# Performance work log

Measured on AMD Instinct MI355X. Metric: run time of the kernel, lower is better.

## Reference

```python
import jax, jax.numpy as jnp
import numpy as np

NUM_HEADS = 16


def setup_inputs() -> dict:
    key = jax.random.key(0)
    k1, k2, k3 = jax.random.split(key, 3)
    B, N, C = 2, 2048, 1024
    x = jax.random.normal(k1, (B, N, C), dtype=jnp.float32)
    w_qkv = jax.random.normal(k2, (3 * C, C), dtype=jnp.float32) * (C ** -0.5)
    w_proj = jax.random.normal(k3, (C, C), dtype=jnp.float32) * (C ** -0.5)
    b_proj = jnp.zeros((C,), dtype=jnp.float32)
    return {"x": x, "w_qkv": w_qkv, "w_proj": w_proj, "b_proj": b_proj}


def reference(x, w_qkv, w_proj, b_proj):
    B, N, C = x.shape
    H = NUM_HEADS
    D = C // H
    scale = 1.0 / jnp.sqrt(jnp.asarray(D, x.dtype))
    qkv = (x @ w_qkv.T).reshape(B, N, 3, H, D)
    qkv = jnp.transpose(qkv, (2, 0, 3, 1, 4))  # [3,B,H,N,D]
    q, k, v = qkv[0], qkv[1], qkv[2]
    # scaled dot-product attention with explicit score matrix [B,H,N,N]
    attn = jnp.einsum('bhnd,bhmd->bhnm', q, k) * scale
    attn = jax.nn.softmax(attn, axis=-1)
    out = jnp.einsum('bhnm,bhmd->bhnd', attn, v)
    out = jnp.transpose(out, (0, 2, 1, 3)).reshape(B, N, C)
    # output projection
    return out @ w_proj.T + b_proj
```

## Files before the change

### kernel.cpp

```cpp
#include <hip/hip_runtime.h>

typedef unsigned short u16;
typedef __attribute__((ext_vector_type(8))) short bf16x8;
typedef __attribute__((ext_vector_type(4))) float f32x4;

#define B_ 2
#define N_ 2048
#define C_ 1024
#define H_ 16
#define D_ 64
#define M_ (B_ * N_)

#define QSCALE 0.18033688011114336f

#define EXP2R(x) __builtin_amdgcn_exp2f(x)

__device__ __forceinline__ u16 f2bf(float f) {
    union { float f; unsigned u; } x; x.f = f;
    return (u16)((x.u + 0x8000u) >> 16);
}
__device__ __forceinline__ unsigned pack2bf(float a, float b) {
    union { float f; unsigned u; } x, y; x.f = a; y.f = b;
    return __builtin_amdgcn_perm(y.u + 0x8000u, x.u + 0x8000u, 0x07060302);
}

__device__ __forceinline__ void async_copy16(const void* gsrc, void* ldst) {
    __builtin_amdgcn_global_load_lds(
        (__attribute__((address_space(1))) void*)gsrc,
        (__attribute__((address_space(3))) void*)ldst,
        16, 0, 0);
}

__global__ void cast3_kernel(const float* __restrict__ x, const float* __restrict__ wq,
                             const float* __restrict__ wp, u16* __restrict__ xo,
                             u16* __restrict__ wqo, u16* __restrict__ wpo) {
    int b = blockIdx.x;
    const float* s; u16* d;
    if (b < 4096)      { s = x;  d = xo;  }
    else if (b < 7168) { s = wq; d = wqo; b -= 4096; }
    else               { s = wp; d = wpo; b -= 7168; }
    int i = (b * 256 + threadIdx.x) * 4;
    const float4 v = *(const float4*)(s + i);
    uint2 o;
    o.x = pack2bf(v.x, v.y);
    o.y = pack2bf(v.z, v.w);
    *(uint2*)(d + i) = o;
}

template <int EPI>
__global__ __launch_bounds__(256, 3) void gemm_bt(
    const u16* __restrict__ A, const u16* __restrict__ Bm,
    int M, int Ncols, int K, int ntiles_n,
    u16* __restrict__ qo, u16* __restrict__ ko, u16* __restrict__ vt,
    const float* __restrict__ bias, float* __restrict__ out) {
    __shared__ u16 As[128 * 64];
    __shared__ u16 Bs[128 * 64];
    const int tid = threadIdx.x, lane = tid & 63, w = tid >> 6;
    const int cpx = gridDim.x >> 3;
    const int sbid = (blockIdx.x & 7) * cpx + (blockIdx.x >> 3);
    const int bx = sbid % ntiles_n, by = sbid / ntiles_n;
    const int m0 = by * 128, n0 = bx * 128;
    const int wm = w >> 1, wn = w & 1;
    const int q16 = lane >> 4, l15 = lane & 15;
    const int r0 = lane >> 3, c0 = (lane & 7) * 8;
    f32x4 acc[4][4] = {};

    for (int k0 = 0; k0 < K; k0 += 64) {
#pragma unroll
        for (int i = 0; i < 4; ++i) {
            int blk = w * 4 + i;
            int r = blk * 8 + r0;
            async_copy16(A + (size_t)(m0 + r) * K + k0 + c0, (char*)As + blk * 1024);
            async_copy16(Bm + (size_t)(n0 + r) * K + k0 + c0, (char*)Bs + blk * 1024);
        }
        __builtin_amdgcn_s_waitcnt(0);
        __syncthreads();
#pragma unroll
        for (int ks = 0; ks < 2; ++ks) {
            bf16x8 af[4], bf[4];
#pragma unroll
            for (int i = 0; i < 4; ++i) {
                af[i] = *(const bf16x8*)&As[(wm * 64 + i * 16 + l15) * 64 + ks * 32 + q16 * 8];
                bf[i] = *(const bf16x8*)&Bs[(wn * 64 + i * 16 + l15) * 64 + ks * 32 + q16 * 8];
            }
#pragma unroll
            for (int mi = 0; mi < 4; ++mi)
#pragma unroll
                for (int ni = 0; ni < 4; ++ni)
                    acc[mi][ni] = __builtin_amdgcn_mfma_f32_16x16x32_bf16(af[mi], bf[ni], acc[mi][ni], 0, 0, 0);
        }
        __syncthreads();
    }

#pragma unroll
    for (int mi = 0; mi < 4; ++mi) {
#pragma unroll
        for (int ni = 0; ni < 4; ++ni) {
            int n_g = n0 + wn * 64 + ni * 16 + l15;
            if (EPI == 0) {
                int which = n_g >> 10;
                int h = (n_g >> 6) & 15;
                int d = n_g & 63;
                int m_base = m0 + wm * 64 + mi * 16 + q16 * 4;
                int b = m_base >> 11;
                int nn0 = m_base & 2047;
                if (which == 2) {
                    uint2 pk;
                    pk.x = pack2bf(acc[mi][ni][0], acc[mi][ni][1]);
                    pk.y = pack2bf(acc[mi][ni][2], acc[mi][ni][3]);
                    *(uint2*)(vt + ((size_t)((b * H_ + h) * D_ + d) << 11) + nn0) = pk;
                } else {
                    size_t base = ((size_t)((b * H_ + h) * N_ + nn0) << 6) + d;
#pragma unroll
                    for (int r = 0; r < 4; ++r) {
                        float v = acc[mi][ni][r];
                        if (which == 0) qo[base + (size_t)r * D_] = f2bf(v * QSCALE);
                        else            ko[base + (size_t)r * D_] = f2bf(v);
                    }
                }
            } else {
#pragma unroll
                for (int r = 0; r < 4; ++r) {
                    int m_g = m0 + wm * 64 + mi * 16 + q16 * 4 + r;
                    out[(size_t)m_g * Ncols + n_g] = acc[mi][ni][r] + bias[n_g];
                }
            }
        }
    }
}

__global__ __launch_bounds__(512, 4) void attn_kernel(
    const u16* __restrict__ Q, const u16* __restrict__ K,
    const u16* __restrict__ VT, u16* __restrict__ O) {
    __shared__ u16 Ks[2][2][64 * 64];
    __shared__ u16 Vs[2][2][64 * 64];
    __shared__ u16 Ps[8][16 * 64];
    const int tid = threadIdx.x, lane = tid & 63, w = tid >> 6;
    const int q16 = lane >> 4, l15 = lane & 15;
    const int l7 = l15 & 7;
    const int bid = blockIdx.x;
    const int bh = (bid & 7) * 4 + (bid >> 7);
    const int q0 = ((bid >> 3) & 15) * 128;
    const size_t head = (size_t)bh * N_ * D_;
    const int lr3 = lane >> 3, lc7 = lane & 7;

    auto stage = [&](int kt, int buf) {
        int key0 = kt * 128;
        int row = w * 8 + lr3;
#pragma unroll
        for (int s = 0; s < 2; ++s) {
            async_copy16(K + head + (size_t)(key0 + s * 64 + row) * D_ + (lc7 ^ lr3) * 8,
                         (char*)Ks[buf][s] + w * 1024);
            async_copy16(VT + head + (size_t)row * N_ + key0 + s * 64 + (lc7 ^ lr3) * 8,
                         (char*)Vs[buf][s] + w * 1024);
        }
    };

    bf16x8 qf[2];
#pragma unroll
    for (int ks = 0; ks < 2; ++ks)
        qf[ks] = *(const bf16x8*)(Q + head + (size_t)(q0 + w * 16 + l15) * D_ + ks * 32 + q16 * 8);
    stage(0, 0);
    __builtin_amdgcn_s_waitcnt(0);
    __syncthreads();

    f32x4 o_acc[4] = {};
    float rs = 0.f;

    for (int kt = 0; kt < 16; ++kt) {
        int buf = kt & 1;
        stage((kt + 1) & 15, buf ^ 1);

#pragma unroll
        for (int s = 0; s < 2; ++s) {
#pragma unroll
            for (int kb = 0; kb < 4; ++kb) {
                f32x4 st = {};
                __builtin_amdgcn_s_setprio(1);
#pragma unroll
                for (int ks = 0; ks < 2; ++ks) {
                    bf16x8 kf = *(const bf16x8*)&Ks[buf][s][(kb * 16 + l15) * 64 + ((ks * 4 + q16) ^ l7) * 8];
                    st = __builtin_amdgcn_mfma_f32_16x16x32_bf16(kf, qf[ks], st, 0, 0, 0);
                }
                __builtin_amdgcn_s_setprio(0);
                float p0 = EXP2R(st[0]), p1 = EXP2R(st[1]);
                float p2 = EXP2R(st[2]), p3 = EXP2R(st[3]);
                rs += (p0 + p1) + (p2 + p3);
                uint2 pk;
                pk.x = pack2bf(p0, p1);
                pk.y = pack2bf(p2, p3);
                int bw = kb * 2 + (q16 >> 1), h = q16 & 1;
                *(uint2*)&Ps[w][l15 * 64 + ((bw ^ l7) * 8 + h * 4)] = pk;
            }

            __builtin_amdgcn_s_setprio(1);
#pragma unroll
            for (int ks2 = 0; ks2 < 2; ++ks2) {
                int br = ks2 * 4 + q16;
                bf16x8 pf = *(const bf16x8*)&Ps[w][l15 * 64 + (br ^ l7) * 8];
#pragma unroll
                for (int di = 0; di < 4; ++di) {
                    bf16x8 vf = *(const bf16x8*)&Vs[buf][s][(di * 16 + l15) * 64 + ((ks2 * 4 + q16) ^ l7) * 8];
                    o_acc[di] = __builtin_amdgcn_mfma_f32_16x16x32_bf16(pf, vf, o_acc[di], 0, 0, 0);
                }
            }
            __builtin_amdgcn_s_setprio(0);
        }

        __builtin_amdgcn_s_waitcnt(0);
        __syncthreads();
    }

    rs += __shfl_xor(rs, 16);
    rs += __shfl_xor(rs, 32);
    float inv[4];
#pragma unroll
    for (int r = 0; r < 4; ++r) inv[r] = 1.0f / __shfl(rs, q16 * 4 + r);

    const int b = bh >> 4, h = bh & 15;
#pragma unroll
    for (int di = 0; di < 4; ++di) {
        int d = di * 16 + l15;
#pragma unroll
        for (int r = 0; r < 4; ++r) {
            int qg = q0 + w * 16 + q16 * 4 + r;
            O[((size_t)(b * N_ + qg) << 10) + h * 64 + d] = f2bf(o_acc[di][r] * inv[r]);
        }
    }
}

extern "C" void kernel_launch(void* const* d_in, const int* in_sizes, int n_in,
                              void* d_out, int out_size, void* d_ws, size_t ws_size,
                              hipStream_t stream) {
    const float* x      = (const float*)d_in[0];
    const float* w_qkv  = (const float*)d_in[1];
    const float* w_proj = (const float*)d_in[2];
    const float* b_proj = (const float*)d_in[3];
    float* out = (float*)d_out;

    char* ws = (char*)d_ws;
    const size_t MB = 1024 * 1024;
    u16* x_bf     = (u16*)(ws + 0 * MB);
    u16* wqkv_bf  = (u16*)(ws + 8 * MB);
    u16* wproj_bf = (u16*)(ws + 14 * MB);
    u16* q_bf     = (u16*)(ws + 16 * MB);
    u16* k_bf     = (u16*)(ws + 24 * MB);
    u16* vt_bf    = (u16*)(ws + 32 * MB);
    u16* ao_bf    = (u16*)(ws + 40 * MB);

    cast3_kernel<<<8192, 256, 0, stream>>>(x, w_qkv, w_proj, x_bf, wqkv_bf, wproj_bf);

    gemm_bt<0><<<32 * 24, 256, 0, stream>>>(x_bf, wqkv_bf, M_, 3 * C_, C_, 24,
                                            q_bf, k_bf, vt_bf, nullptr, nullptr);

    attn_kernel<<<512, 512, 0, stream>>>(q_bf, k_bf, vt_bf, ao_bf);

    gemm_bt<1><<<32 * 8, 256, 0, stream>>>(ao_bf, wproj_bf, M_, C_, C_, 8,
                                           nullptr, nullptr, nullptr, b_proj, out);
}
```

Baseline: 186.7 us.

## Process two query sub-tiles per wave in attention to reuse K/V fragments

Each wave now handles 32 query rows (two 16-row sub-tiles), so every K and V fragment read from LDS feeds two MFMAs. Blocks cover 256 queries, which halves the grid to 256 blocks, and launch bounds are relaxed to allow more registers. This cuts LDS reads and global K/V staging per unit of work. In exchange it costs more registers and fewer resident blocks, which reduces latency hiding and CU balance.

```diff
diff --git a/kernel.cpp b/kernel.cpp
--- a/kernel.cpp
+++ b/kernel.cpp
@@ -129,18 +129,18 @@
     }
 }
 
-__global__ __launch_bounds__(512, 4) void attn_kernel(
+__global__ __launch_bounds__(512, 1) void attn_kernel(
     const u16* __restrict__ Q, const u16* __restrict__ K,
     const u16* __restrict__ VT, u16* __restrict__ O) {
     __shared__ u16 Ks[2][2][64 * 64];
     __shared__ u16 Vs[2][2][64 * 64];
-    __shared__ u16 Ps[8][16 * 64];
+    __shared__ u16 Ps[8][2][16 * 64];
     const int tid = threadIdx.x, lane = tid & 63, w = tid >> 6;
     const int q16 = lane >> 4, l15 = lane & 15;
     const int l7 = l15 & 7;
     const int bid = blockIdx.x;
-    const int bh = (bid & 7) * 4 + (bid >> 7);
-    const int q0 = ((bid >> 3) & 15) * 128;
+    const int bh = (bid & 7) * 4 + (bid >> 6);
+    const int q0 = ((bid >> 3) & 7) * 256;
     const size_t head = (size_t)bh * N_ * D_;
     const int lr3 = lane >> 3, lc7 = lane & 7;
 
@@ -156,16 +156,19 @@
         }
     };
 
-    bf16x8 qf[2];
-#pragma unroll
-    for (int ks = 0; ks < 2; ++ks)
-        qf[ks] = *(const bf16x8*)(Q + head + (size_t)(q0 + w * 16 + l15) * D_ + ks * 32 + q16 * 8);
+    bf16x8 qf[2][2];
+#pragma unroll
+    for (int qh = 0; qh < 2; ++qh)
+#pragma unroll
+        for (int ks = 0; ks < 2; ++ks)
+            qf[qh][ks] = *(const bf16x8*)(Q + head +
+                (size_t)(q0 + w * 32 + qh * 16 + l15) * D_ + ks * 32 + q16 * 8);
     stage(0, 0);
     __builtin_amdgcn_s_waitcnt(0);
     __syncthreads();
 
-    f32x4 o_acc[4] = {};
-    float rs = 0.f;
+    f32x4 o_acc[2][4] = {};
+    float rs[2] = {0.f, 0.f};
 
     for (int kt = 0; kt < 16; ++kt) {
         int buf = kt & 1;
@@ -175,33 +178,44 @@
         for (int s = 0; s < 2; ++s) {
 #pragma unroll
             for (int kb = 0; kb < 4; ++kb) {
-                f32x4 st = {};
+                bf16x8 kf[2];
+#pragma unroll
+                for (int ks = 0; ks < 2; ++ks)
+                    kf[ks] = *(const bf16x8*)&Ks[buf][s][(kb * 16 + l15) * 64 + ((ks * 4 + q16) ^ l7) * 8];
+                f32x4 st[2] = {};
                 __builtin_amdgcn_s_setprio(1);
 #pragma unroll
                 for (int ks = 0; ks < 2; ++ks) {
-                    bf16x8 kf = *(const bf16x8*)&Ks[buf][s][(kb * 16 + l15) * 64 + ((ks * 4 + q16) ^ l7) * 8];
-                    st = __builtin_amdgcn_mfma_f32_16x16x32_bf16(kf, qf[ks], st, 0, 0, 0);
+                    st[0] = __builtin_amdgcn_mfma_f32_16x16x32_bf16(kf[ks], qf[0][ks], st[0], 0, 0, 0);
+                    st[1] = __builtin_amdgcn_mfma_f32_16x16x32_bf16(kf[ks], qf[1][ks], st[1], 0, 0, 0);
                 }
                 __builtin_amdgcn_s_setprio(0);
-                float p0 = EXP2R(st[0]), p1 = EXP2R(st[1]);
-                float p2 = EXP2R(st[2]), p3 = EXP2R(st[3]);
-                rs += (p0 + p1) + (p2 + p3);
-                uint2 pk;
-                pk.x = pack2bf(p0, p1);
-                pk.y = pack2bf(p2, p3);
                 int bw = kb * 2 + (q16 >> 1), h = q16 & 1;
-                *(uint2*)&Ps[w][l15 * 64 + ((bw ^ l7) * 8 + h * 4)] = pk;
+#pragma unroll
+                for (int qh = 0; qh < 2; ++qh) {
+                    float p0 = EXP2R(st[qh][0]), p1 = EXP2R(st[qh][1]);
+                    float p2 = EXP2R(st[qh][2]), p3 = EXP2R(st[qh][3]);
+                    rs[qh] += (p0 + p1) + (p2 + p3);
+                    uint2 pk;
+                    pk.x = pack2bf(p0, p1);
+                    pk.y = pack2bf(p2, p3);
+                    *(uint2*)&Ps[w][qh][l15 * 64 + ((bw ^ l7) * 8 + h * 4)] = pk;
+                }
             }
 
             __builtin_amdgcn_s_setprio(1);
 #pragma unroll
             for (int ks2 = 0; ks2 < 2; ++ks2) {
                 int br = ks2 * 4 + q16;
-                bf16x8 pf = *(const bf16x8*)&Ps[w][l15 * 64 + (br ^ l7) * 8];
+                bf16x8 pf[2];
+#pragma unroll
+                for (int qh = 0; qh < 2; ++qh)
+                    pf[qh] = *(const bf16x8*)&Ps[w][qh][l15 * 64 + (br ^ l7) * 8];
 #pragma unroll
                 for (int di = 0; di < 4; ++di) {
                     bf16x8 vf = *(const bf16x8*)&Vs[buf][s][(di * 16 + l15) * 64 + ((ks2 * 4 + q16) ^ l7) * 8];
-                    o_acc[di] = __builtin_amdgcn_mfma_f32_16x16x32_bf16(pf, vf, o_acc[di], 0, 0, 0);
+                    o_acc[0][di] = __builtin_amdgcn_mfma_f32_16x16x32_bf16(pf[0], vf, o_acc[0][di], 0, 0, 0);
+                    o_acc[1][di] = __builtin_amdgcn_mfma_f32_16x16x32_bf16(pf[1], vf, o_acc[1][di], 0, 0, 0);
                 }
             }
             __builtin_amdgcn_s_setprio(0);
@@ -211,20 +225,22 @@
         __syncthreads();
     }
 
-    rs += __shfl_xor(rs, 16);
-    rs += __shfl_xor(rs, 32);
-    float inv[4];
-#pragma unroll
-    for (int r = 0; r < 4; ++r) inv[r] = 1.0f / __shfl(rs, q16 * 4 + r);
-
     const int b = bh >> 4, h = bh & 15;
 #pragma unroll
-    for (int di = 0; di < 4; ++di) {
-        int d = di * 16 + l15;
-#pragma unroll
-        for (int r = 0; r < 4; ++r) {
-            int qg = q0 + w * 16 + q16 * 4 + r;
-            O[((size_t)(b * N_ + qg) << 10) + h * 64 + d] = f2bf(o_acc[di][r] * inv[r]);
+    for (int qh = 0; qh < 2; ++qh) {
+        rs[qh] += __shfl_xor(rs[qh], 16);
+        rs[qh] += __shfl_xor(rs[qh], 32);
+        float inv[4];
+#pragma unroll
+        for (int r = 0; r < 4; ++r) inv[r] = 1.0f / __shfl(rs[qh], q16 * 4 + r);
+#pragma unroll
+        for (int di = 0; di < 4; ++di) {
+            int d = di * 16 + l15;
+#pragma unroll
+            for (int r = 0; r < 4; ++r) {
+                int qg = q0 + w * 32 + qh * 16 + q16 * 4 + r;
+                O[((size_t)(b * N_ + qg) << 10) + h * 64 + d] = f2bf(o_acc[qh][di][r] * inv[r]);
+            }
         }
     }
 }
@@ -253,7 +269,7 @@
     gemm_bt<0><<<32 * 24, 256, 0, stream>>>(x_bf, wqkv_bf, M_, 3 * C_, C_, 24,
                                             q_bf, k_bf, vt_bf, nullptr, nullptr);
 
-    attn_kernel<<<512, 512, 0, stream>>>(q_bf, k_bf, vt_bf, ao_bf);
+    attn_kernel<<<256, 512, 0, stream>>>(q_bf, k_bf, vt_bf, ao_bf);
 
     gemm_bt<1><<<32 * 8, 256, 0, stream>>>(ao_bf, wproj_bf, M_, C_, C_, 8,
                                            nullptr, nullptr, nullptr, b_proj, out);
```

Measured after the change: 188.0 us. No clear change (+0.7%).

## Switch attention to 32x32x16 MFMA with register-resident P via permlane32 swap

Applied to the files above, without the earlier changes.

Rewrites the attention inner loop to use 32x32x16 bf16 MFMA tiles, with each wave handling 32 query rows and each block 256 queries, so the grid is halved to 256 blocks. The softmax probabilities are packed and rearranged across half-waves with v_permlane32_swap, so P feeds the PV MFMA directly from registers and the LDS Ps buffer and its round trip go away. The trade-off is higher register pressure (launch bounds relaxed to 1) and fewer blocks, which may underfill the GPU's compute units.

```diff
diff --git a/kernel.cpp b/kernel.cpp
--- a/kernel.cpp
+++ b/kernel.cpp
@@ -3,6 +3,8 @@
 typedef unsigned short u16;
 typedef __attribute__((ext_vector_type(8))) short bf16x8;
 typedef __attribute__((ext_vector_type(4))) float f32x4;
+typedef __attribute__((ext_vector_type(16))) float f32x16;
+typedef __attribute__((ext_vector_type(4))) unsigned u32x4;
 
 #define B_ 2
 #define N_ 2048
@@ -129,18 +131,16 @@
     }
 }
 
-__global__ __launch_bounds__(512, 4) void attn_kernel(
+__global__ __launch_bounds__(512, 1) void attn_kernel(
     const u16* __restrict__ Q, const u16* __restrict__ K,
     const u16* __restrict__ VT, u16* __restrict__ O) {
     __shared__ u16 Ks[2][2][64 * 64];
     __shared__ u16 Vs[2][2][64 * 64];
-    __shared__ u16 Ps[8][16 * 64];
     const int tid = threadIdx.x, lane = tid & 63, w = tid >> 6;
-    const int q16 = lane >> 4, l15 = lane & 15;
-    const int l7 = l15 & 7;
+    const int l31 = lane & 31, hi = lane >> 5, l7 = l31 & 7;
     const int bid = blockIdx.x;
-    const int bh = (bid & 7) * 4 + (bid >> 7);
-    const int q0 = ((bid >> 3) & 15) * 128;
+    const int bh = (bid & 7) * 4 + (bid >> 6);
+    const int q0 = ((bid >> 3) & 7) * 256;
     const size_t head = (size_t)bh * N_ * D_;
     const int lr3 = lane >> 3, lc7 = lane & 7;
 
@@ -156,15 +156,15 @@
         }
     };
 
-    bf16x8 qf[2];
-#pragma unroll
-    for (int ks = 0; ks < 2; ++ks)
-        qf[ks] = *(const bf16x8*)(Q + head + (size_t)(q0 + w * 16 + l15) * D_ + ks * 32 + q16 * 8);
+    bf16x8 qf[4];
+#pragma unroll
+    for (int ds = 0; ds < 4; ++ds)
+        qf[ds] = *(const bf16x8*)(Q + head + (size_t)(q0 + w * 32 + l31) * D_ + ds * 16 + hi * 8);
     stage(0, 0);
     __builtin_amdgcn_s_waitcnt(0);
     __syncthreads();
 
-    f32x4 o_acc[4] = {};
+    f32x16 o_acc[2] = {};
     float rs = 0.f;
 
     for (int kt = 0; kt < 16; ++kt) {
@@ -174,57 +174,63 @@
 #pragma unroll
         for (int s = 0; s < 2; ++s) {
 #pragma unroll
-            for (int kb = 0; kb < 4; ++kb) {
-                f32x4 st = {};
+            for (int kb2 = 0; kb2 < 2; ++kb2) {
+                f32x16 st = {};
                 __builtin_amdgcn_s_setprio(1);
 #pragma unroll
-                for (int ks = 0; ks < 2; ++ks) {
-                    bf16x8 kf = *(const bf16x8*)&Ks[buf][s][(kb * 16 + l15) * 64 + ((ks * 4 + q16) ^ l7) * 8];
-                    st = __builtin_amdgcn_mfma_f32_16x16x32_bf16(kf, qf[ks], st, 0, 0, 0);
+                for (int ds = 0; ds < 4; ++ds) {
+                    bf16x8 kf = *(const bf16x8*)&Ks[buf][s][(kb2 * 32 + l31) * 64 + ((ds * 2 + hi) ^ l7) * 8];
+                    st = __builtin_amdgcn_mfma_f32_32x32x16_bf16(kf, qf[ds], st, 0, 0, 0);
                 }
                 __builtin_amdgcn_s_setprio(0);
-                float p0 = EXP2R(st[0]), p1 = EXP2R(st[1]);
-                float p2 = EXP2R(st[2]), p3 = EXP2R(st[3]);
-                rs += (p0 + p1) + (p2 + p3);
-                uint2 pk;
-                pk.x = pack2bf(p0, p1);
-                pk.y = pack2bf(p2, p3);
-                int bw = kb * 2 + (q16 >> 1), h = q16 & 1;
-                *(uint2*)&Ps[w][l15 * 64 + ((bw ^ l7) * 8 + h * 4)] = pk;
+
+                float p[16];
+#pragma unroll
+                for (int i = 0; i < 16; ++i) p[i] = EXP2R(st[i]);
+#pragma unroll
+                for (int i = 0; i < 16; ++i) rs += p[i];
+
+                unsigned a0 = pack2bf(p[0], p[1]),   b0 = pack2bf(p[4], p[5]);
+                unsigned a1 = pack2bf(p[2], p[3]),   b1 = pack2bf(p[6], p[7]);
+                unsigned a2 = pack2bf(p[8], p[9]),   b2 = pack2bf(p[12], p[13]);
+                unsigned a3 = pack2bf(p[10], p[11]), b3 = pack2bf(p[14], p[15]);
+                asm("v_permlane32_swap_b32 %0, %1" : "+v"(a0), "+v"(b0));
+                asm("v_permlane32_swap_b32 %0, %1" : "+v"(a1), "+v"(b1));
+                asm("v_permlane32_swap_b32 %0, %1" : "+v"(a2), "+v"(b2));
+                asm("v_permlane32_swap_b32 %0, %1" : "+v"(a3), "+v"(b3));
+                union { u32x4 u; bf16x8 v; } af0, af1;
+                af0.u = (u32x4){a0, a1, b0, b1};
+                af1.u = (u32x4){a2, a3, b2, b3};
+
+                __builtin_amdgcn_s_setprio(1);
+#pragma unroll
+                for (int db = 0; db < 2; ++db) {
+                    bf16x8 vf0 = *(const bf16x8*)&Vs[buf][s][(db * 32 + l31) * 64 + ((kb2 * 4 + hi) ^ l7) * 8];
+                    o_acc[db] = __builtin_amdgcn_mfma_f32_32x32x16_bf16(af0.v, vf0, o_acc[db], 0, 0, 0);
+                    bf16x8 vf1 = *(const bf16x8*)&Vs[buf][s][(db * 32 + l31) * 64 + ((kb2 * 4 + 2 + hi) ^ l7) * 8];
+                    o_acc[db] = __builtin_amdgcn_mfma_f32_32x32x16_bf16(af1.v, vf1, o_acc[db], 0, 0, 0);
+                }
+                __builtin_amdgcn_s_setprio(0);
             }
-
-            __builtin_amdgcn_s_setprio(1);
-#pragma unroll
-            for (int ks2 = 0; ks2 < 2; ++ks2) {
-                int br = ks2 * 4 + q16;
-                bf16x8 pf = *(const bf16x8*)&Ps[w][l15 * 64 + (br ^ l7) * 8];
-#pragma unroll
-                for (int di = 0; di < 4; ++di) {
-                    bf16x8 vf = *(const bf16x8*)&Vs[buf][s][(di * 16 + l15) * 64 + ((ks2 * 4 + q16) ^ l7) * 8];
-                    o_acc[di] = __builtin_amdgcn_mfma_f32_16x16x32_bf16(pf, vf, o_acc[di], 0, 0, 0);
-                }
-            }
-            __builtin_amdgcn_s_setprio(0);
         }
 
         __builtin_amdgcn_s_waitcnt(0);
         __syncthreads();
     }
 
-    rs += __shfl_xor(rs, 16);
     rs += __shfl_xor(rs, 32);
-    float inv[4];
-#pragma unroll
-    for (int r = 0; r < 4; ++r) inv[r] = 1.0f / __shfl(rs, q16 * 4 + r);
+    float rsi = 1.0f / rs;
 
     const int b = bh >> 4, h = bh & 15;
 #pragma unroll
-    for (int di = 0; di < 4; ++di) {
-        int d = di * 16 + l15;
-#pragma unroll
-        for (int r = 0; r < 4; ++r) {
-            int qg = q0 + w * 16 + q16 * 4 + r;
-            O[((size_t)(b * N_ + qg) << 10) + h * 64 + d] = f2bf(o_acc[di][r] * inv[r]);
+    for (int reg = 0; reg < 16; ++reg) {
+        int qrow = (reg & 3) + 8 * (reg >> 2) + 4 * hi;
+        float inv = __shfl(rsi, qrow);
+        int qg = q0 + w * 32 + qrow;
+#pragma unroll
+        for (int db = 0; db < 2; ++db) {
+            int d = db * 32 + l31;
+            O[((size_t)(b * N_ + qg) << 10) + h * 64 + d] = f2bf(o_acc[db][reg] * inv);
         }
     }
 }
@@ -253,7 +259,7 @@
     gemm_bt<0><<<32 * 24, 256, 0, stream>>>(x_bf, wqkv_bf, M_, 3 * C_, C_, 24,
                                             q_bf, k_bf, vt_bf, nullptr, nullptr);
 
-    attn_kernel<<<512, 512, 0, stream>>>(q_bf, k_bf, vt_bf, ao_bf);
+    attn_kernel<<<256, 512, 0, stream>>>(q_bf, k_bf, vt_bf, ao_bf);
 
     gemm_bt<1><<<32 * 8, 256, 0, stream>>>(ao_bf, wproj_bf, M_, C_, C_, 8,
                                            nullptr, nullptr, nullptr, b_proj, out);
```

Result: faster. 181.7 us (-2.7%).
